# Kernel optimization log

Hardware: AMD Instinct MI355X
Metric: run time of the kernel (lower is better)

Reference implementation:

```python
import jax, jax.numpy as jnp
import numpy as np

B, L, A = 16, 32, 2046
M = A + 2  # user col + attributors + item col = 2048 nodes


def _xavier_uniform(key, shape, gain):
    fan_out, fan_in = shape  # torch 2D param: fan_in = shape[1], fan_out = shape[0]
    bound = gain * np.sqrt(6.0 / (fan_in + fan_out))
    return jax.random.uniform(key, shape, jnp.float32, -bound, bound)


def setup_inputs() -> dict:
    key = jax.random.key(0)
    k = jax.random.split(key, 7)
    user = jax.random.normal(k[0], (B, 6 * L, 1), jnp.float32)
    item = jax.random.normal(k[1], (B, 6 * L, 1), jnp.float32)
    attributor = jax.random.normal(k[2], (B, 6 * L, A), jnp.float32)
    adj = (jax.random.uniform(k[3], (M, M)) < 0.5).astype(jnp.float32)
    initial_weight = jax.random.normal(k[4], (M, M), jnp.float32)
    W_1 = _xavier_uniform(k[5], (6 * L, A), gain=np.sqrt(2.0))  # relu gain
    W_2 = _xavier_uniform(k[6], (6 * L, L), gain=1.44)
    return {"user": user, "item": item, "attributor": attributor,
            "adj": adj, "initial_weight": initial_weight,
            "W_1": W_1, "W_2": W_2}


def reference(user, item, attributor, adj, initial_weight, W_1, W_2):
    N = W_2.shape[1]  # = length L
    a = attributor * W_1                                   # (B, 6L, A)
    raw = jnp.concatenate([user, a, item], axis=2)         # (B, 6L, M)
    Q, K, V = jnp.split(raw, 3, axis=1)                    # each (B, 2L, M)
    r = jax.nn.relu
    # (relu(X).T @ W).T  ==  einsum over the 2L dim -> (B, L, M)
    Query = jnp.einsum('bnm,nl->blm', r(Q), W_2[:2 * N])
    Key = jnp.einsum('bnm,nl->blm', r(K), W_2[2 * N:4 * N])
    Value = jnp.einsum('bnm,nl->blm', r(V), W_2[4 * N:])
    # h = Query.mT @ Key * adj * initial_weight  -> (B, M, M)
    h = jnp.einsum('blm,bln->bmn', Query, Key) * adj * initial_weight
    d = h - jnp.swapaxes(h, -1, -2)
    exp_h = jnp.exp(jnp.where(d > 0, 0.0, d))              # exp(min(d, 0))
    causal = exp_h / (exp_h + jnp.swapaxes(exp_h, -1, -2)) * adj  # (B, M, M)
    Ans = Value @ causal                                    # (B, L, M)
    idx = jnp.array([0, Ans.shape[2] - 1])
    return Ans[:, :, idx]                                   # (B, L, 2)
```

## Files before the change

### kernel.cpp

```cpp
#include <hip/hip_runtime.h>
#include <math.h>

#define BB 16
#define LL 32
#define AA 2046
#define MM 2048
#define NROWS 192
#define CT 64
#define CPB 32


__global__ __launch_bounds__(256) void fused_kernel(
    const float* __restrict__ user, const float* __restrict__ item,
    const float* __restrict__ att, const float* __restrict__ adj,
    const float* __restrict__ iw, const float* __restrict__ W1,
    const float* __restrict__ W2, float* __restrict__ out) {
  const int ctile = blockIdx.x, b = blockIdx.y, tid = threadIdx.x;
  __shared__ float KQ[4][LL];
  __shared__ float uvs[4][64];
  __shared__ float stS[32][8][4][2];
  __shared__ float cs[2][CPB];
  __shared__ float gred[32][2][2];

  if (tid < 128) {
    const int q = tid >> 5, l = tid & 31;
    const float* __restrict__ src = (q == 0 || q == 2) ? user : item;
    const int rbase = (q < 2) ? 64 : 0;
    float acc = 0.f;
#pragma unroll
    for (int r = 0; r < 64; ++r)
      acc += fmaxf(src[b * NROWS + rbase + r], 0.f) * W2[(rbase + r) * LL + l];
    KQ[q][l] = acc;
  }
  __syncthreads();
  {
    const int which = tid >> 6, r = tid & 63;
    const int wrow = (which < 2) ? r : 64 + r;
    float acc = 0.f;
#pragma unroll
    for (int l = 0; l < LL; ++l) acc += W2[wrow * LL + l] * KQ[which][l];
    uvs[which][r] = acc;
  }
  __syncthreads();

  const int cq = tid & 7, rg = tid >> 3;
  const int c0 = ctile * CPB + cq * 4;
  const bool tail = (c0 + 2 >= AA);

  float vst[4][4];
  float vva[2][4];
  const int sbase = (rg < 16) ? 0 : 64;
  const int r0 = sbase + (rg & 15) * 4;
#pragma unroll
  for (int i = 0; i < 4; ++i) {
    const int r = r0 + i;
    const size_t arow = (size_t)(b * NROWS + r) * AA;
    const size_t wrow = (size_t)r * AA;
    const float2 av0 = *(const float2*)(att + arow + c0);
    const float2 wv0 = *(const float2*)(W1 + wrow + c0);
    vst[i][0] = fmaxf(av0.x * wv0.x, 0.f);
    vst[i][1] = fmaxf(av0.y * wv0.y, 0.f);
    if (!tail) {
      const float2 av1 = *(const float2*)(att + arow + c0 + 2);
      const float2 wv1 = *(const float2*)(W1 + wrow + c0 + 2);
      vst[i][2] = fmaxf(av1.x * wv1.x, 0.f);
      vst[i][3] = fmaxf(av1.y * wv1.y, 0.f);
    } else {
      vst[i][2] = fmaxf(user[b * NROWS + r], 0.f);
      vst[i][3] = fmaxf(item[b * NROWS + r], 0.f);
    }
  }
#pragma unroll
  for (int i = 0; i < 2; ++i) {
    const int r = 128 + rg * 2 + i;
    const size_t arow = (size_t)(b * NROWS + r) * AA;
    const size_t wrow = (size_t)r * AA;
    const float2 av0 = *(const float2*)(att + arow + c0);
    const float2 wv0 = *(const float2*)(W1 + wrow + c0);
    vva[i][0] = fmaxf(av0.x * wv0.x, 0.f);
    vva[i][1] = fmaxf(av0.y * wv0.y, 0.f);
    if (!tail) {
      const float2 av1 = *(const float2*)(att + arow + c0 + 2);
      const float2 wv1 = *(const float2*)(W1 + wrow + c0 + 2);
      vva[i][2] = fmaxf(av1.x * wv1.x, 0.f);
      vva[i][3] = fmaxf(av1.y * wv1.y, 0.f);
    } else {
      vva[i][2] = fmaxf(user[b * NROWS + r], 0.f);
      vva[i][3] = fmaxf(item[b * NROWS + r], 0.f);
    }
  }

  {
    const float* __restrict__ wj0 = uvs[(rg < 16) ? 0 : 2];
    const float* __restrict__ wj1 = uvs[(rg < 16) ? 1 : 3];
    float a[4][2] = {};
#pragma unroll
    for (int i = 0; i < 4; ++i) {
      const int widx = (rg & 15) * 4 + i;
      const float u0 = wj0[widx], u1 = wj1[widx];
#pragma unroll
      for (int k = 0; k < 4; ++k) {
        a[k][0] += vst[i][k] * u0;
        a[k][1] += vst[i][k] * u1;
      }
    }
#pragma unroll
    for (int k = 0; k < 4; ++k) {
      stS[rg][cq][k][0] = a[k][0];
      stS[rg][cq][k][1] = a[k][1];
    }
  }
  __syncthreads();

  if (tid < 64) {
    const int col = tid >> 1, j = tid & 1;
    const int q = col >> 2, ci = col & 3;
    float s = 0.f, t = 0.f;
#pragma unroll
    for (int g = 0; g < 16; ++g) s += stS[g][q][ci][j];
#pragma unroll
    for (int g = 16; g < 32; ++g) t += stS[g][q][ci][j];
    const int cc = ctile * CPB + col;
    const int n = (cc < AA) ? cc + 1 : ((cc == AA) ? 0 : MM - 1);
    const size_t tcol = j ? (MM - 1) : 0;
    const float an = adj[(size_t)n * MM + tcol];
    const float wn = an * iw[(size_t)n * MM + tcol];
    const float wt = adj[tcol * MM + n] * iw[tcol * MM + n];
    const float d = s * wn - t * wt;
    const float e = expf(-fabsf(d));
    const float sig = (d > 0.f) ? 1.f / (1.f + e) : e / (1.f + e);
    cs[j][col] = sig * an;
  }
  __syncthreads();

  {
    float g[2][2];
#pragma unroll
    for (int i = 0; i < 2; ++i) {
      g[i][0] = vva[i][0] * cs[0][cq * 4] + vva[i][1] * cs[0][cq * 4 + 1] +
                vva[i][2] * cs[0][cq * 4 + 2] + vva[i][3] * cs[0][cq * 4 + 3];
      g[i][1] = vva[i][0] * cs[1][cq * 4] + vva[i][1] * cs[1][cq * 4 + 1] +
                vva[i][2] * cs[1][cq * 4 + 2] + vva[i][3] * cs[1][cq * 4 + 3];
    }
#pragma unroll
    for (int m = 4; m >= 1; m >>= 1) {
#pragma unroll
      for (int i = 0; i < 2; ++i) {
        g[i][0] += __shfl_xor(g[i][0], m, 8);
        g[i][1] += __shfl_xor(g[i][1], m, 8);
      }
    }
    if (cq == 0) {
#pragma unroll
      for (int i = 0; i < 2; ++i) {
        gred[rg][i][0] = g[i][0];
        gred[rg][i][1] = g[i][1];
      }
    }
  }
  __syncthreads();

  if (tid < 64) {
    const int l = tid & 31, j = tid >> 5;
    float acc = 0.f;
#pragma unroll
    for (int rv = 0; rv < 64; ++rv)
      acc += W2[(128 + rv) * LL + l] * gred[rv >> 1][rv & 1][j];
    atomicAdd(&out[b * (LL * 2) + l * 2 + j], acc);
  }
}

extern "C" void kernel_launch(void* const* d_in, const int* in_sizes, int n_in,
                              void* d_out, int out_size, void* d_ws,
                              size_t ws_size, hipStream_t stream) {
  const float* user = (const float*)d_in[0];
  const float* item = (const float*)d_in[1];
  const float* att = (const float*)d_in[2];
  const float* adj = (const float*)d_in[3];
  const float* iw = (const float*)d_in[4];
  const float* W1 = (const float*)d_in[5];
  const float* W2 = (const float*)d_in[6];
  float* out = (float*)d_out;

  hipMemsetAsync(d_out, 0, sizeof(float) * (size_t)out_size, stream);
  fused_kernel<<<dim3(CT, BB), 256, 0, stream>>>(user, item, att, adj, iw, W1,
                                                 W2, out);
}
```

Baseline: 111.9 us.

## Halve columns per block, double grid, and defer V-row loads until needed

Each block now covers 16 columns instead of 32, so the grid doubles to 128x16 blocks and each thread handles 2 columns with one float2 load per row. The value rows are no longer loaded up front. They are read after the causal weights are computed, which lowers register pressure. The intent is more parallelism and better latency hiding for this memory-bound kernel. The cost is that the per-block KQ/uvs prologue and the atomics are duplicated across twice as many blocks, and the V loads are no longer overlapped with the earlier phase.

Measured after the change: 119.0 us. 6.3% more time.

```diff
diff --git a/kernel.cpp b/kernel.cpp
--- a/kernel.cpp
+++ b/kernel.cpp
@@ -6,8 +6,8 @@
 #define AA 2046
 #define MM 2048
 #define NROWS 192
-#define CT 64
-#define CPB 32
+#define CT 128
+#define CPB 16
 
 
 __global__ __launch_bounds__(256) void fused_kernel(
@@ -18,9 +18,13 @@
   const int ctile = blockIdx.x, b = blockIdx.y, tid = threadIdx.x;
   __shared__ float KQ[4][LL];
   __shared__ float uvs[4][64];
-  __shared__ float stS[32][8][4][2];
+  __shared__ float stS[32][8][2][2];
   __shared__ float cs[2][CPB];
   __shared__ float gred[32][2][2];
+
+  const int cq = tid & 7, rg = tid >> 3;
+  const int c0 = ctile * CPB + cq * 2;
+  const bool tail = (c0 >= AA);
 
   if (tid < 128) {
     const int q = tid >> 5, l = tid & 31;
@@ -43,78 +47,40 @@
   }
   __syncthreads();
 
-  const int cq = tid & 7, rg = tid >> 3;
-  const int c0 = ctile * CPB + cq * 4;
-  const bool tail = (c0 + 2 >= AA);
-
-  float vst[4][4];
-  float vva[2][4];
-  const int sbase = (rg < 16) ? 0 : 64;
-  const int r0 = sbase + (rg & 15) * 4;
-#pragma unroll
-  for (int i = 0; i < 4; ++i) {
-    const int r = r0 + i;
-    const size_t arow = (size_t)(b * NROWS + r) * AA;
-    const size_t wrow = (size_t)r * AA;
-    const float2 av0 = *(const float2*)(att + arow + c0);
-    const float2 wv0 = *(const float2*)(W1 + wrow + c0);
-    vst[i][0] = fmaxf(av0.x * wv0.x, 0.f);
-    vst[i][1] = fmaxf(av0.y * wv0.y, 0.f);
-    if (!tail) {
-      const float2 av1 = *(const float2*)(att + arow + c0 + 2);
-      const float2 wv1 = *(const float2*)(W1 + wrow + c0 + 2);
-      vst[i][2] = fmaxf(av1.x * wv1.x, 0.f);
-      vst[i][3] = fmaxf(av1.y * wv1.y, 0.f);
-    } else {
-      vst[i][2] = fmaxf(user[b * NROWS + r], 0.f);
-      vst[i][3] = fmaxf(item[b * NROWS + r], 0.f);
-    }
-  }
-#pragma unroll
-  for (int i = 0; i < 2; ++i) {
-    const int r = 128 + rg * 2 + i;
-    const size_t arow = (size_t)(b * NROWS + r) * AA;
-    const size_t wrow = (size_t)r * AA;
-    const float2 av0 = *(const float2*)(att + arow + c0);
-    const float2 wv0 = *(const float2*)(W1 + wrow + c0);
-    vva[i][0] = fmaxf(av0.x * wv0.x, 0.f);
-    vva[i][1] = fmaxf(av0.y * wv0.y, 0.f);
-    if (!tail) {
-      const float2 av1 = *(const float2*)(att + arow + c0 + 2);
-      const float2 wv1 = *(const float2*)(W1 + wrow + c0 + 2);
-      vva[i][2] = fmaxf(av1.x * wv1.x, 0.f);
-      vva[i][3] = fmaxf(av1.y * wv1.y, 0.f);
-    } else {
-      vva[i][2] = fmaxf(user[b * NROWS + r], 0.f);
-      vva[i][3] = fmaxf(item[b * NROWS + r], 0.f);
-    }
-  }
-
   {
     const float* __restrict__ wj0 = uvs[(rg < 16) ? 0 : 2];
     const float* __restrict__ wj1 = uvs[(rg < 16) ? 1 : 3];
-    float a[4][2] = {};
+    const int rbase = (rg < 16) ? 0 : 64;
+    const int rrow0 = (rg & 15) * 4 + rbase;
+    float a[2][2] = {};
 #pragma unroll
     for (int i = 0; i < 4; ++i) {
-      const int widx = (rg & 15) * 4 + i;
+      const int r = rrow0 + i;
+      const int widx = r - rbase;
+      float v0, v1;
+      if (!tail) {
+        const float2 av =
+            *(const float2*)(att + (size_t)(b * NROWS + r) * AA + c0);
+        const float2 wv = *(const float2*)(W1 + (size_t)r * AA + c0);
+        v0 = fmaxf(av.x * wv.x, 0.f);
+        v1 = fmaxf(av.y * wv.y, 0.f);
+      } else {
+        v0 = fmaxf(user[b * NROWS + r], 0.f);
+        v1 = fmaxf(item[b * NROWS + r], 0.f);
+      }
       const float u0 = wj0[widx], u1 = wj1[widx];
-#pragma unroll
-      for (int k = 0; k < 4; ++k) {
-        a[k][0] += vst[i][k] * u0;
-        a[k][1] += vst[i][k] * u1;
-      }
+      a[0][0] += v0 * u0;
+      a[0][1] += v0 * u1;
+      a[1][0] += v1 * u0;
+      a[1][1] += v1 * u1;
     }
-#pragma unroll
-    for (int k = 0; k < 4; ++k) {
-      stS[rg][cq][k][0] = a[k][0];
-      stS[rg][cq][k][1] = a[k][1];
-    }
+    *(float4*)&stS[rg][cq][0][0] = make_float4(a[0][0], a[0][1], a[1][0], a[1][1]);
   }
   __syncthreads();
 
-  if (tid < 64) {
+  if (tid < 32) {
     const int col = tid >> 1, j = tid & 1;
-    const int q = col >> 2, ci = col & 3;
+    const int q = col >> 1, ci = col & 1;
     float s = 0.f, t = 0.f;
 #pragma unroll
     for (int g = 0; g < 16; ++g) s += stS[g][q][ci][j];
@@ -134,13 +100,25 @@
   __syncthreads();
 
   {
+    const float c00 = cs[0][cq * 2], c01 = cs[0][cq * 2 + 1];
+    const float c10 = cs[1][cq * 2], c11 = cs[1][cq * 2 + 1];
     float g[2][2];
 #pragma unroll
     for (int i = 0; i < 2; ++i) {
-      g[i][0] = vva[i][0] * cs[0][cq * 4] + vva[i][1] * cs[0][cq * 4 + 1] +
-                vva[i][2] * cs[0][cq * 4 + 2] + vva[i][3] * cs[0][cq * 4 + 3];
-      g[i][1] = vva[i][0] * cs[1][cq * 4] + vva[i][1] * cs[1][cq * 4 + 1] +
-                vva[i][2] * cs[1][cq * 4 + 2] + vva[i][3] * cs[1][cq * 4 + 3];
+      const int r = 128 + rg * 2 + i;
+      float v0, v1;
+      if (!tail) {
+        const float2 av =
+            *(const float2*)(att + (size_t)(b * NROWS + r) * AA + c0);
+        const float2 wv = *(const float2*)(W1 + (size_t)r * AA + c0);
+        v0 = fmaxf(av.x * wv.x, 0.f);
+        v1 = fmaxf(av.y * wv.y, 0.f);
+      } else {
+        v0 = fmaxf(user[b * NROWS + r], 0.f);
+        v1 = fmaxf(item[b * NROWS + r], 0.f);
+      }
+      g[i][0] = v0 * c00 + v1 * c01;
+      g[i][1] = v0 * c10 + v1 * c11;
     }
 #pragma unroll
     for (int m = 4; m >= 1; m >>= 1) {
```
